# Optimization experiments

Hardware: AMD Instinct MI355X
Metric: run time of the kernel (lower is better)

The kernel has to match this reference:

```python
import jax, jax.numpy as jnp
import numpy as np

SCORE_THRESH = 0.05
NMS_THRESH = 0.5
K = 1000            # max NMS candidates (fixed for jit; padded/masked)
IMG_W, IMG_H = 1333, 800


def setup_inputs() -> dict:
    key = jax.random.key(0)
    k1, k2, k3 = jax.random.split(key, 3)
    N, C = 200000, 81
    class_logits = jax.random.normal(k1, (N, C), dtype=jnp.float32) * 2.0
    # well-formed xyxy boxes inside the image
    cxcy = jax.random.uniform(k2, (N, 2), dtype=jnp.float32) * jnp.array([IMG_W, IMG_H], jnp.float32)
    wh = jax.random.uniform(k3, (N, 2), dtype=jnp.float32) * 200.0 + 1.0
    boxes = jnp.concatenate([cxcy - wh * 0.5, cxcy + wh * 0.5], axis=-1)
    return {"class_logits": class_logits, "boxes": boxes}


def _pairwise_iou(b):
    # b: [K, 4] xyxy -> [K, K]
    area = (b[:, 2] - b[:, 0]) * (b[:, 3] - b[:, 1])
    lt = jnp.maximum(b[:, None, :2], b[None, :, :2])
    rb = jnp.minimum(b[:, None, 2:], b[None, :, 2:])
    wh = jnp.clip(rb - lt, 0.0)
    inter = wh[..., 0] * wh[..., 1]
    return inter / (area[:, None] + area[None, :] - inter + 1e-9)


def reference(class_logits, boxes):
    N, C = class_logits.shape
    prob = jax.nn.softmax(class_logits, axis=-1)            # [N, C]
    # clip_to_image (TO_REMOVE=1 convention: clamp to size-1)
    bx = jnp.stack([
        jnp.clip(boxes[:, 0], 0.0, IMG_W - 1),
        jnp.clip(boxes[:, 1], 0.0, IMG_H - 1),
        jnp.clip(boxes[:, 2], 0.0, IMG_W - 1),
        jnp.clip(boxes[:, 3], 0.0, IMG_H - 1),
    ], axis=-1)                                             # [N, 4]
    flat = prob.reshape(-1)                                 # [N*C], class = idx % C
    idx = jnp.arange(N * C)
    valid = (flat > SCORE_THRESH) & (idx % C != 0)          # fg + score threshold
    masked = jnp.where(valid, flat, -jnp.inf)
    top_scores, top_idx = jax.lax.top_k(masked, K)          # sorted descending
    prop_idx = top_idx // C
    cls = top_idx % C
    bk = bx[prop_idx]                                       # [K, 4]
    valid_k = jnp.isfinite(top_scores)
    scores_k = jnp.where(valid_k, top_scores, 0.0)
    # class-aware greedy NMS over the (sorted) top-K candidates
    conflict = (_pairwise_iou(bk) > NMS_THRESH) & (cls[:, None] == cls[None, :])
    rng = jnp.arange(K)

    def body(i, keep):
        sup = jnp.any(keep & conflict[:, i] & (rng < i))
        return keep.at[i].set(keep[i] & ~sup)

    keep = jax.lax.fori_loop(0, K, body, valid_k)
    out = jnp.concatenate([bk, scores_k[:, None]], axis=-1) * keep[:, None].astype(bk.dtype)
    return out  # [K, 5]: (x1, y1, x2, y2, score), zeroed where suppressed/invalid
```

## Files before the change

kernel.cpp:

```cpp
#include <hip/hip_runtime.h>
#include <stdint.h>
#include <math.h>

#define N_CLS    81
#define TOPK     1000
#define LISTCAP  (1u << 21)
#define CAP2     16384
#define SCORE_TH 0.05f
#define IMG_W    1333.0f
#define IMG_H    800.0f
#define GH_REP   8

#define GH_BASE  1905

#define OFF_CNT    0
#define OFF_CNT2   8
#define OFF_GH     64
#define OFF_RH     4608
#define OFF_SORTED 8704
#define MEMSET_BYTES 16704
#define OFF_SEL    16768
#define OFF_SEL2   16793984
#define OFF_BOX    16925056
#define OFF_SCORE  16941056
#define OFF_CLS    16945056
#define OFF_MASK   16949056

#define ROWS_PER_BLK 128
#define TILE_FLOATS  (ROWS_PER_BLK * N_CLS)
#define CBUF_CAP     1024

typedef unsigned long long u64;

__device__ __forceinline__ void gload_lds16(const float* g, float* l) {
    __builtin_amdgcn_global_load_lds(
        (const __attribute__((address_space(1))) unsigned int*)g,
        (__attribute__((address_space(3))) unsigned int*)l, 16, 0, 0);
}

__global__ __launch_bounds__(256) void k_pass1(
        const float* __restrict__ logits, int nrows,
        u64* __restrict__ sel, unsigned* __restrict__ cnt,
        unsigned* __restrict__ ghist) {
    __shared__ float tile[TILE_FLOATS];
    __shared__ unsigned lh[128];
    __shared__ u64 cbuf[CBUF_CAP];
    __shared__ unsigned lcnt, gbase;
    int tid = threadIdx.x, wv = tid >> 6, ln = tid & 63;
    for (int i = tid; i < 128; i += 256) lh[i] = 0;
    if (tid == 0) lcnt = 0;

    int base = blockIdx.x * ROWS_PER_BLK;
    int nr = nrows - base; if (nr > ROWS_PER_BLK) nr = ROWS_PER_BLK;
    const float* gtile = logits + (size_t)base * N_CLS;

    if (nr == ROWS_PER_BLK) {
        #pragma unroll
        for (int it = 0; it < 10; ++it) {
            int c = it * 1024 + wv * 256;
            gload_lds16(gtile + c + ln * 4, tile + c);
        }
        if (tid < TILE_FLOATS - 10240) tile[10240 + tid] = gtile[10240 + tid];
    } else {
        for (int i = tid; i < nr * N_CLS; i += 256) tile[i] = gtile[i];
    }
    __syncthreads();

    int r = tid >> 1, h = tid & 1;
    if (r < nr) {
        const int rb = r * N_CLS + h;
        float v[41];
        #pragma unroll
        for (int m = 0; m < 40; ++m) v[m] = tile[rb + 2 * m];
        v[40] = (h == 0) ? tile[rb + 80] : 0.0f;

        float mx = v[0];
        #pragma unroll
        for (int m = 1; m < 40; ++m) mx = fmaxf(mx, v[m]);
        mx = fmaxf(mx, (h == 0) ? v[40] : v[0]);
        float om = __shfl_xor(mx, 1);
        float mrow = fmaxf(mx, om);

        #pragma unroll
        for (int m = 0; m < 40; ++m) v[m] = expf(v[m] - mrow);
        v[40] = (h == 0) ? expf(v[40] - mrow) : 0.0f;

        float stk0 = 0.f, stk1 = 0.f, stk2 = 0.f, stk3 = 0.f, stk4 = 0.f;
        float S = 0.f;
        #pragma unroll
        for (int i = 0; i < 32; ++i) {
            const int b = ((i & 1) << 4) | ((i & 2) << 2) | (i & 4) |
                          ((i & 8) >> 2) | ((i & 16) >> 4);
            float x = v[b];
            if (b < 8) x += v[b + 32];
            else if (b == 8) x = (h == 0) ? x + v[40] : x;
            if (i & 1) { x = stk0 + x;
              if (i & 2) { x = stk1 + x;
                if (i & 4) { x = stk2 + x;
                  if (i & 8) { x = stk3 + x;
                    if (i & 16) { S = stk4 + x; } else stk4 = x;
                  } else stk3 = x;
                } else stk2 = x;
              } else stk1 = x;
            } else stk0 = x;
        }
        float oS = __shfl_xor(S, 1);
        float s = (h == 0) ? (S + oS) : (oS + S);

        float eth = 0.0499f * s;
        unsigned rowflat = (unsigned)(base + r) * N_CLS + (unsigned)h;
        #pragma unroll
        for (int m = 0; m < 41; ++m) {
            float e = v[m];
            if ((m + h) != 0 && e > eth) {
                float p = e / s;
                if (p > SCORE_TH) {
                    unsigned fb = __float_as_uint(p);
                    atomicAdd(&lh[(fb >> 19) - GH_BASE], 1u);
                    unsigned flat = rowflat + 2u * (unsigned)m;
                    u64 key = ((u64)fb << 32) | (u64)(0xFFFFFFu - flat);
                    unsigned pos = atomicAdd(&lcnt, 1u);
                    if (pos < CBUF_CAP) cbuf[pos] = key;
                    else { unsigned gp = atomicAdd(cnt, 1u); if (gp < LISTCAP) sel[gp] = key; }
                }
            }
        }
    }
    __syncthreads();
    unsigned* gh = ghist + (blockIdx.x & (GH_REP - 1)) * 128;
    for (int i = tid; i < 128; i += 256) {
        unsigned vv = lh[i];
        if (vv) atomicAdd(&gh[i], vv);
    }
    unsigned total = lcnt; if (total > CBUF_CAP) total = CBUF_CAP;
    if (tid == 0) gbase = atomicAdd(cnt, total);
    __syncthreads();
    unsigned gb = gbase;
    for (unsigned i = tid; i < total; i += 256) {
        unsigned gp = gb + i;
        if (gp < LISTCAP) sel[gp] = cbuf[i];
    }
}

__device__ inline int scan_coarse(const unsigned* __restrict__ ghist, unsigned* c_above) {
    unsigned cum = 0;
    for (int i = 127; i >= 0; --i) {
        unsigned c = 0;
        #pragma unroll
        for (int r = 0; r < GH_REP; r++) c += ghist[r * 128 + i];
        if (cum + c >= TOPK) { *c_above = cum; return i; }
        cum += c;
    }
    *c_above = cum;
    return -1;
}

__global__ __launch_bounds__(256) void k_refine(
        const u64* __restrict__ sel, const unsigned* __restrict__ cnt,
        const unsigned* __restrict__ ghist, unsigned* __restrict__ rhist) {
    __shared__ unsigned lh[1024];
    __shared__ int sB;
    int tid = threadIdx.x;
    for (int i = tid; i < 1024; i += 256) lh[i] = 0;
    if (tid == 0) { unsigned ca; sB = scan_coarse(ghist, &ca); }
    __syncthreads();
    int B = sB;
    if (B < 0) return;
    unsigned Bbits = (unsigned)(B + GH_BASE);
    unsigned M = *cnt; if (M > LISTCAP) M = LISTCAP;
    unsigned stride = gridDim.x * blockDim.x;
    for (unsigned i = blockIdx.x * blockDim.x + tid; i < M; i += stride) {
        unsigned bits = (unsigned)(sel[i] >> 32);
        if ((bits >> 19) == Bbits) atomicAdd(&lh[(bits >> 9) & 1023u], 1u);
    }
    __syncthreads();
    for (int i = tid; i < 1024; i += 256) {
        unsigned v = lh[i];
        if (v) atomicAdd(&rhist[i], v);
    }
}

__global__ __launch_bounds__(256) void k_select(
        const u64* __restrict__ sel, const unsigned* __restrict__ cnt,
        const unsigned* __restrict__ ghist, const unsigned* __restrict__ rhist,
        u64* __restrict__ sel2, unsigned* __restrict__ cnt2) {
    __shared__ unsigned s4[256];
    __shared__ unsigned tbs;
    int tid = threadIdx.x, ln = tid & 63;
    unsigned ps = 0;
    #pragma unroll
    for (int k = 0; k < 4; k++) ps += rhist[tid * 4 + k];
    s4[tid] = ps;
    __syncthreads();
    if (tid == 0) {
        unsigned c_above;
        int B = scan_coarse(ghist, &c_above);
        unsigned tb = 0;
        if (B >= 0) {
            unsigned cab = c_above;
            int g = -1;
            for (int i = 255; i >= 0; --i) {
                if (cab + s4[i] >= TOPK) { g = i; break; }
                cab += s4[i];
            }
            int sb = 0;
            if (g >= 0) {
                for (int i = g * 4 + 3; i >= g * 4; --i) {
                    unsigned c = rhist[i];
                    if (cab + c >= TOPK) { sb = i; break; }
                    cab += c;
                }
            }
            tb = ((unsigned)(B + GH_BASE) << 19) | ((unsigned)sb << 9);
        }
        tbs = tb;
    }
    __syncthreads();
    unsigned tb = tbs;
    unsigned M = *cnt; if (M > LISTCAP) M = LISTCAP;
    unsigned stride = gridDim.x * blockDim.x;
    for (unsigned ibase = blockIdx.x * blockDim.x; ibase < M; ibase += stride) {
        unsigned i = ibase + tid;
        bool act = (i < M);
        u64 key = act ? sel[i] : 0ull;
        bool c = act && ((unsigned)(key >> 32) >= tb);
        u64 b = __ballot(c);
        int n = __popcll(b);
        if (n == 0) continue;
        unsigned wb = 0;
        if (ln == 0) wb = atomicAdd(cnt2, (unsigned)n);
        wb = __shfl(wb, 0);
        if (c) {
            unsigned pos = wb + (unsigned)__popcll(b & ((1ull << ln) - 1ull));
            if (pos < CAP2) sel2[pos] = key;
        }
    }
}

__global__ __launch_bounds__(256) void k_rank(
        const u64* __restrict__ sel2, const unsigned* __restrict__ cnt2,
        u64* __restrict__ sorted) {
    __shared__ u64 ch[2048];
    unsigned S = *cnt2; if (S > CAP2) S = CAP2;
    if (blockIdx.x * 256u >= S) return;
    unsigned t = blockIdx.x * 256u + threadIdx.x;
    u64 my = (t < S) ? sel2[t] : 0ull;
    int r = 0;
    for (unsigned c0 = 0; c0 < S; c0 += 2048) {
        unsigned n = S - c0; if (n > 2048) n = 2048;
        __syncthreads();
        for (unsigned i = threadIdx.x; i < n; i += 256) ch[i] = sel2[c0 + i];
        __syncthreads();
        if (t < S)
            for (unsigned j = 0; j < n; j++) r += (ch[j] > my) ? 1 : 0;
    }
    if (t < S && r < TOPK) sorted[r] = my;
}

__global__ __launch_bounds__(256) void k_decode(
        const u64* __restrict__ sorted, const float* __restrict__ boxes,
        float* __restrict__ boxK, float* __restrict__ scoreK, int* __restrict__ clsK) {
    int t = blockIdx.x * blockDim.x + threadIdx.x;
    if (t >= TOPK) return;
    u64 key = sorted[t];
    if (key != 0ull) {
        float sc = __uint_as_float((unsigned)(key >> 32));
        unsigned fi = 0xFFFFFFu - (unsigned)(key & 0xFFFFFFFFull);
        unsigned prop = fi / N_CLS;
        int cls = (int)(fi - prop * N_CLS);
        const float* b = boxes + (size_t)prop * 4;
        boxK[t * 4 + 0] = fminf(fmaxf(b[0], 0.0f), IMG_W - 1.0f);
        boxK[t * 4 + 1] = fminf(fmaxf(b[1], 0.0f), IMG_H - 1.0f);
        boxK[t * 4 + 2] = fminf(fmaxf(b[2], 0.0f), IMG_W - 1.0f);
        boxK[t * 4 + 3] = fminf(fmaxf(b[3], 0.0f), IMG_H - 1.0f);
        scoreK[t] = sc;
        clsK[t] = cls;
    } else {
        boxK[t * 4 + 0] = 0.0f; boxK[t * 4 + 1] = 0.0f;
        boxK[t * 4 + 2] = 0.0f; boxK[t * 4 + 3] = 0.0f;
        scoreK[t] = 0.0f;
        clsK[t] = -1;
    }
}

__global__ __launch_bounds__(256) void k_conflict(
        const float* __restrict__ boxK, const int* __restrict__ clsK,
        u64* __restrict__ mask) {
    int t = blockIdx.x * blockDim.x + threadIdx.x;
    if (t >= TOPK * 16) return;
    int i = t >> 4, w = t & 15;
    float x1 = boxK[i * 4 + 0], y1 = boxK[i * 4 + 1];
    float x2 = boxK[i * 4 + 2], y2 = boxK[i * 4 + 3];
    int ci = clsK[i];
    float ai = (x2 - x1) * (y2 - y1);
    u64 m = 0;
    int jbase = w << 6;
    for (int jj = 0; jj < 64; jj++) {
        int j = jbase + jj;
        if (j >= TOPK) break;
        float u1 = boxK[j * 4 + 0], w1 = boxK[j * 4 + 1];
        float u2 = boxK[j * 4 + 2], w2 = boxK[j * 4 + 3];
        float aj = (u2 - u1) * (w2 - w1);
        float ww = fmaxf(fminf(x2, u2) - fmaxf(x1, u1), 0.0f);
        float hh = fmaxf(fminf(y2, w2) - fmaxf(y1, w1), 0.0f);
        float inter = ww * hh;
        float iou = inter / (ai + aj - inter + 1e-9f);
        if (iou > 0.5f && ci == clsK[j]) m |= (1ull << jj);
    }
    mask[(size_t)i * 16 + w] = m;
}

__global__ __launch_bounds__(1024) void k_nms_out(
        const u64* __restrict__ mask, const float* __restrict__ boxK,
        const float* __restrict__ scoreK, float* __restrict__ out) {
    __shared__ u64 words[16];
    __shared__ int changed;
    int tid = threadIdx.x, wv = tid >> 6, ln = tid & 63;
    bool valid = (tid < TOPK) && (scoreK[tid] > 0.0f);
    u64 row[16];
    #pragma unroll
    for (int w = 0; w < 16; w++)
        row[w] = (tid < TOPK) ? mask[(size_t)tid * 16 + w] : 0ull;
    u64 lowmask = (1ull << ln) - 1ull;
    bool keep = valid;
    for (int it = 0; it < 1024; ++it) {
        u64 b = __ballot(keep);
        if (ln == 0) words[wv] = b;
        if (tid == 0) changed = 0;
        __syncthreads();
        u64 sup = 0;
        for (int w = 0; w <= wv; w++) {
            u64 kw = words[w];
            if (w == wv) kw &= lowmask;
            sup |= row[w] & kw;
        }
        bool nk = valid && (sup == 0ull);
        if (nk != keep) changed = 1;
        keep = nk;
        __syncthreads();
        if (!changed) break;
    }
    if (tid < TOPK) {
        float x1 = boxK[tid * 4 + 0], y1 = boxK[tid * 4 + 1];
        float x2 = boxK[tid * 4 + 2], y2 = boxK[tid * 4 + 3];
        float sc = scoreK[tid];
        out[tid * 5 + 0] = keep ? x1 : 0.0f;
        out[tid * 5 + 1] = keep ? y1 : 0.0f;
        out[tid * 5 + 2] = keep ? x2 : 0.0f;
        out[tid * 5 + 3] = keep ? y2 : 0.0f;
        out[tid * 5 + 4] = keep ? sc : 0.0f;
    }
}

extern "C" void kernel_launch(void* const* d_in, const int* in_sizes, int n_in,
                              void* d_out, int out_size, void* d_ws, size_t ws_size,
                              hipStream_t stream) {
    const float* logits = (const float*)d_in[0];
    const float* boxes  = (const float*)d_in[1];
    float* out = (float*)d_out;
    int nrows = in_sizes[0] / N_CLS;

    char* w = (char*)d_ws;
    unsigned* cnt    = (unsigned*)(w + OFF_CNT);
    unsigned* cnt2   = (unsigned*)(w + OFF_CNT2);
    unsigned* ghist  = (unsigned*)(w + OFF_GH);
    unsigned* rhist  = (unsigned*)(w + OFF_RH);
    u64* sorted      = (u64*)(w + OFF_SORTED);
    u64* sel         = (u64*)(w + OFF_SEL);
    u64* sel2        = (u64*)(w + OFF_SEL2);
    float* boxK      = (float*)(w + OFF_BOX);
    float* scoreK    = (float*)(w + OFF_SCORE);
    int* clsK        = (int*)(w + OFF_CLS);
    u64* mask        = (u64*)(w + OFF_MASK);

    hipMemsetAsync(w, 0, MEMSET_BYTES, stream);

    int nblk = (nrows + ROWS_PER_BLK - 1) / ROWS_PER_BLK;
    k_pass1<<<nblk, 256, 0, stream>>>(logits, nrows, sel, cnt, ghist);
    k_refine<<<256, 256, 0, stream>>>(sel, cnt, ghist, rhist);
    k_select<<<256, 256, 0, stream>>>(sel, cnt, ghist, rhist, sel2, cnt2);
    k_rank<<<CAP2 / 256, 256, 0, stream>>>(sel2, cnt2, sorted);
    k_decode<<<(TOPK + 255) / 256, 256, 0, stream>>>(sorted, boxes, boxK, scoreK, clsK);
    k_conflict<<<(TOPK * 16 + 255) / 256, 256, 0, stream>>>(boxK, clsK, mask);
    k_nms_out<<<1, 1024, 0, stream>>>(mask, boxK, scoreK, out);
}
```

Measured before the change: 200.3 us.

## Fold threshold scans into last-block epilogues and fuse rank with decode

Pass1 now uses 64-row blocks of 128 threads and records survivors as a per-thread bitmask. A wave-wide prefix scan assigns global write positions with one atomic per wave, replacing the LDS candidate buffer. The last-arriving block of pass1 and of refine, picked with a ticket counter, computes the coarse bin and the threshold with parallel scans, so k_refine and k_select no longer rescan the histograms serially in thread 0. The rank and decode kernels are merged into one, which removes a launch and the sorted buffer. The conflict kernel now reads boxes as float4. The ticket scheme relies on threadfence ordering, and the smaller blocks roughly double the block count.

```diff
diff --git a/kernel.cpp b/kernel.cpp
--- a/kernel.cpp
+++ b/kernel.cpp
@@ -15,10 +15,14 @@
 
 #define OFF_CNT    0
 #define OFF_CNT2   8
+#define OFF_TICK1  16
+#define OFF_TICK2  20
+#define OFF_SB     24
+#define OFF_CA     28
+#define OFF_TB     32
 #define OFF_GH     64
 #define OFF_RH     4608
-#define OFF_SORTED 8704
-#define MEMSET_BYTES 16704
+#define MEMSET_BYTES 8704
 #define OFF_SEL    16768
 #define OFF_SEL2   16793984
 #define OFF_BOX    16925056
@@ -26,9 +30,8 @@
 #define OFF_CLS    16945056
 #define OFF_MASK   16949056
 
-#define ROWS_PER_BLK 128
+#define ROWS_PER_BLK 64
 #define TILE_FLOATS  (ROWS_PER_BLK * N_CLS)
-#define CBUF_CAP     1024
 
 typedef unsigned long long u64;
 
@@ -38,17 +41,21 @@
         (__attribute__((address_space(3))) unsigned int*)l, 16, 0, 0);
 }
 
-__global__ __launch_bounds__(256) void k_pass1(
+__device__ __forceinline__ unsigned agent_load_u32(const unsigned* p) {
+    return __hip_atomic_load(p, __ATOMIC_RELAXED, __HIP_MEMORY_SCOPE_AGENT);
+}
+
+__global__ __launch_bounds__(128) void k_pass1(
         const float* __restrict__ logits, int nrows,
         u64* __restrict__ sel, unsigned* __restrict__ cnt,
-        unsigned* __restrict__ ghist) {
+        unsigned* __restrict__ ghist, unsigned* __restrict__ tick,
+        int* __restrict__ psB, unsigned* __restrict__ pCA) {
     __shared__ float tile[TILE_FLOATS];
     __shared__ unsigned lh[128];
-    __shared__ u64 cbuf[CBUF_CAP];
-    __shared__ unsigned lcnt, gbase;
+    __shared__ unsigned scs[128], ssfx[128];
+    __shared__ int wB;
+    __shared__ unsigned wCA, tkt;
     int tid = threadIdx.x, wv = tid >> 6, ln = tid & 63;
-    for (int i = tid; i < 128; i += 256) lh[i] = 0;
-    if (tid == 0) lcnt = 0;
 
     int base = blockIdx.x * ROWS_PER_BLK;
     int nr = nrows - base; if (nr > ROWS_PER_BLK) nr = ROWS_PER_BLK;
@@ -57,19 +64,22 @@
     if (nr == ROWS_PER_BLK) {
         #pragma unroll
         for (int it = 0; it < 10; ++it) {
-            int c = it * 1024 + wv * 256;
+            int c = it * 512 + wv * 256;
             gload_lds16(gtile + c + ln * 4, tile + c);
         }
-        if (tid < TILE_FLOATS - 10240) tile[10240 + tid] = gtile[10240 + tid];
+        if (tid < 64) tile[5120 + tid] = gtile[5120 + tid];
     } else {
-        for (int i = tid; i < nr * N_CLS; i += 256) tile[i] = gtile[i];
-    }
+        for (int i = tid; i < nr * N_CLS; i += 128) tile[i] = gtile[i];
+    }
+    lh[tid] = 0;
     __syncthreads();
 
     int r = tid >> 1, h = tid & 1;
+    float v[41];
+    float s = 1.0f;
+    u64 bits = 0;
     if (r < nr) {
         const int rb = r * N_CLS + h;
-        float v[41];
         #pragma unroll
         for (int m = 0; m < 40; ++m) v[m] = tile[rb + 2 * m];
         v[40] = (h == 0) ? tile[rb + 80] : 0.0f;
@@ -105,118 +115,149 @@
             } else stk0 = x;
         }
         float oS = __shfl_xor(S, 1);
-        float s = (h == 0) ? (S + oS) : (oS + S);
+        s = (h == 0) ? (S + oS) : (oS + S);
 
         float eth = 0.0499f * s;
-        unsigned rowflat = (unsigned)(base + r) * N_CLS + (unsigned)h;
         #pragma unroll
         for (int m = 0; m < 41; ++m) {
             float e = v[m];
             if ((m + h) != 0 && e > eth) {
                 float p = e / s;
-                if (p > SCORE_TH) {
-                    unsigned fb = __float_as_uint(p);
-                    atomicAdd(&lh[(fb >> 19) - GH_BASE], 1u);
-                    unsigned flat = rowflat + 2u * (unsigned)m;
-                    u64 key = ((u64)fb << 32) | (u64)(0xFFFFFFu - flat);
-                    unsigned pos = atomicAdd(&lcnt, 1u);
-                    if (pos < CBUF_CAP) cbuf[pos] = key;
-                    else { unsigned gp = atomicAdd(cnt, 1u); if (gp < LISTCAP) sel[gp] = key; }
-                }
+                if (p > SCORE_TH) bits |= (1ull << m);
             }
         }
     }
-    __syncthreads();
-    unsigned* gh = ghist + (blockIdx.x & (GH_REP - 1)) * 128;
-    for (int i = tid; i < 128; i += 256) {
-        unsigned vv = lh[i];
-        if (vv) atomicAdd(&gh[i], vv);
-    }
-    unsigned total = lcnt; if (total > CBUF_CAP) total = CBUF_CAP;
-    if (tid == 0) gbase = atomicAdd(cnt, total);
-    __syncthreads();
-    unsigned gb = gbase;
-    for (unsigned i = tid; i < total; i += 256) {
-        unsigned gp = gb + i;
-        if (gp < LISTCAP) sel[gp] = cbuf[i];
-    }
-}
-
-__device__ inline int scan_coarse(const unsigned* __restrict__ ghist, unsigned* c_above) {
-    unsigned cum = 0;
-    for (int i = 127; i >= 0; --i) {
-        unsigned c = 0;
-        #pragma unroll
-        for (int r = 0; r < GH_REP; r++) c += ghist[r * 128 + i];
-        if (cum + c >= TOPK) { *c_above = cum; return i; }
-        cum += c;
-    }
-    *c_above = cum;
-    return -1;
+
+    unsigned pc = (unsigned)__popcll(bits);
+    unsigned scan = pc;
+    #pragma unroll
+    for (int off = 1; off < 64; off <<= 1) {
+        unsigned t = __shfl_up(scan, off);
+        if (ln >= off) scan += t;
+    }
+    unsigned wtotal = __shfl(scan, 63);
+    unsigned wbase = 0;
+    if (ln == 63 && wtotal) wbase = atomicAdd(cnt, wtotal);
+    wbase = __shfl(wbase, 63);
+    unsigned pos = wbase + scan - pc;
+    unsigned rowflat = (unsigned)(base + r) * N_CLS + (unsigned)h;
+    while (bits) {
+        int m = (int)(__ffsll((unsigned long long)bits) - 1);
+        bits &= bits - 1;
+        float p = v[m] / s;
+        unsigned fb = __float_as_uint(p);
+        atomicAdd(&lh[(fb >> 19) - GH_BASE], 1u);
+        if (pos < LISTCAP)
+            sel[pos] = ((u64)fb << 32) | (u64)(0xFFFFFFu - (rowflat + 2u * (unsigned)m));
+        pos++;
+    }
+
+    __syncthreads();
+    { unsigned vv = lh[tid];
+      if (vv) atomicAdd(&ghist[(blockIdx.x & (GH_REP - 1)) * 128 + tid], vv); }
+    __threadfence();
+    __syncthreads();
+    if (tid == 0) tkt = atomicAdd(tick, 1u);
+    __syncthreads();
+    if (tkt != gridDim.x - 1) return;
+
+    unsigned c = 0;
+    #pragma unroll
+    for (int rr = 0; rr < GH_REP; ++rr)
+        c += agent_load_u32(&ghist[rr * 128 + tid]);
+    scs[tid] = c; ssfx[tid] = c;
+    if (tid == 0) wB = -1;
+    __syncthreads();
+    #pragma unroll
+    for (int off = 1; off < 128; off <<= 1) {
+        unsigned a = (tid + off < 128) ? ssfx[tid + off] : 0u;
+        __syncthreads();
+        ssfx[tid] += a;
+        __syncthreads();
+    }
+    if (tid == 0) wCA = ssfx[0];
+    __syncthreads();
+    unsigned incl = ssfx[tid], excl = incl - scs[tid];
+    if (excl < TOPK && incl >= TOPK) { wB = tid; wCA = excl; }
+    __syncthreads();
+    if (tid == 0) { *psB = wB; *pCA = wCA; }
 }
 
 __global__ __launch_bounds__(256) void k_refine(
         const u64* __restrict__ sel, const unsigned* __restrict__ cnt,
-        const unsigned* __restrict__ ghist, unsigned* __restrict__ rhist) {
+        unsigned* __restrict__ rhist, unsigned* __restrict__ tick,
+        const int* __restrict__ psB, const unsigned* __restrict__ pCA,
+        unsigned* __restrict__ ptb) {
     __shared__ unsigned lh[1024];
-    __shared__ int sB;
+    __shared__ unsigned rbin[1024];
+    __shared__ unsigned sgrp[256], ssfx[256];
+    __shared__ int wg;
+    __shared__ unsigned wcab, tkt;
     int tid = threadIdx.x;
-    for (int i = tid; i < 1024; i += 256) lh[i] = 0;
-    if (tid == 0) { unsigned ca; sB = scan_coarse(ghist, &ca); }
-    __syncthreads();
-    int B = sB;
-    if (B < 0) return;
-    unsigned Bbits = (unsigned)(B + GH_BASE);
-    unsigned M = *cnt; if (M > LISTCAP) M = LISTCAP;
-    unsigned stride = gridDim.x * blockDim.x;
-    for (unsigned i = blockIdx.x * blockDim.x + tid; i < M; i += stride) {
-        unsigned bits = (unsigned)(sel[i] >> 32);
-        if ((bits >> 19) == Bbits) atomicAdd(&lh[(bits >> 9) & 1023u], 1u);
-    }
-    __syncthreads();
-    for (int i = tid; i < 1024; i += 256) {
-        unsigned v = lh[i];
-        if (v) atomicAdd(&rhist[i], v);
+    int B = *psB;
+    if (B >= 0) {
+        for (int i = tid; i < 1024; i += 256) lh[i] = 0;
+        __syncthreads();
+        unsigned Bbits = (unsigned)(B + GH_BASE);
+        unsigned M = *cnt; if (M > LISTCAP) M = LISTCAP;
+        unsigned stride = gridDim.x * blockDim.x;
+        for (unsigned i = blockIdx.x * blockDim.x + tid; i < M; i += stride) {
+            unsigned bv = (unsigned)(sel[i] >> 32);
+            if ((bv >> 19) == Bbits) atomicAdd(&lh[(bv >> 9) & 1023u], 1u);
+        }
+        __syncthreads();
+        for (int i = tid; i < 1024; i += 256) {
+            unsigned vv = lh[i];
+            if (vv) atomicAdd(&rhist[i], vv);
+        }
+    }
+    __threadfence();
+    __syncthreads();
+    if (tid == 0) tkt = atomicAdd(tick, 1u);
+    __syncthreads();
+    if (tkt != gridDim.x - 1) return;
+
+    if (B < 0) { if (tid == 0) *ptb = 0u; return; }
+    unsigned CA = *pCA;
+    unsigned gsum = 0;
+    #pragma unroll
+    for (int k = 0; k < 4; ++k) {
+        unsigned bv = agent_load_u32(&rhist[tid * 4 + k]);
+        rbin[tid * 4 + k] = bv; gsum += bv;
+    }
+    sgrp[tid] = gsum; ssfx[tid] = gsum;
+    if (tid == 0) wg = -1;
+    __syncthreads();
+    #pragma unroll
+    for (int off = 1; off < 256; off <<= 1) {
+        unsigned a = (tid + off < 256) ? ssfx[tid + off] : 0u;
+        __syncthreads();
+        ssfx[tid] += a;
+        __syncthreads();
+    }
+    unsigned incl = ssfx[tid], excl = incl - sgrp[tid];
+    if (CA + excl < TOPK && CA + incl >= TOPK) { wg = tid; wcab = CA + excl; }
+    __syncthreads();
+    if (tid == 0) {
+        int g = wg; unsigned sb = 0;
+        if (g >= 0) {
+            unsigned cab = wcab;
+            for (int i = g * 4 + 3; i >= g * 4; --i) {
+                unsigned cc = rbin[i];
+                if (cab + cc >= TOPK) { sb = (unsigned)i; break; }
+                cab += cc;
+            }
+        }
+        *ptb = ((unsigned)(B + GH_BASE) << 19) | (sb << 9);
     }
 }
 
 __global__ __launch_bounds__(256) void k_select(
         const u64* __restrict__ sel, const unsigned* __restrict__ cnt,
-        const unsigned* __restrict__ ghist, const unsigned* __restrict__ rhist,
+        const unsigned* __restrict__ ptb,
         u64* __restrict__ sel2, unsigned* __restrict__ cnt2) {
-    __shared__ unsigned s4[256];
-    __shared__ unsigned tbs;
     int tid = threadIdx.x, ln = tid & 63;
-    unsigned ps = 0;
-    #pragma unroll
-    for (int k = 0; k < 4; k++) ps += rhist[tid * 4 + k];
-    s4[tid] = ps;
-    __syncthreads();
-    if (tid == 0) {
-        unsigned c_above;
-        int B = scan_coarse(ghist, &c_above);
-        unsigned tb = 0;
-        if (B >= 0) {
-            unsigned cab = c_above;
-            int g = -1;
-            for (int i = 255; i >= 0; --i) {
-                if (cab + s4[i] >= TOPK) { g = i; break; }
-                cab += s4[i];
-            }
-            int sb = 0;
-            if (g >= 0) {
-                for (int i = g * 4 + 3; i >= g * 4; --i) {
-                    unsigned c = rhist[i];
-                    if (cab + c >= TOPK) { sb = i; break; }
-                    cab += c;
-                }
-            }
-            tb = ((unsigned)(B + GH_BASE) << 19) | ((unsigned)sb << 9);
-        }
-        tbs = tb;
-    }
-    __syncthreads();
-    unsigned tb = tbs;
+    unsigned tb = *ptb;
     unsigned M = *cnt; if (M > LISTCAP) M = LISTCAP;
     unsigned stride = gridDim.x * blockDim.x;
     for (unsigned ibase = blockIdx.x * blockDim.x; ibase < M; ibase += stride) {
@@ -237,13 +278,21 @@
     }
 }
 
-__global__ __launch_bounds__(256) void k_rank(
+__global__ __launch_bounds__(256) void k_rank_decode(
         const u64* __restrict__ sel2, const unsigned* __restrict__ cnt2,
-        u64* __restrict__ sorted) {
+        const float* __restrict__ boxes,
+        float* __restrict__ boxK, float* __restrict__ scoreK, int* __restrict__ clsK) {
     __shared__ u64 ch[2048];
     unsigned S = *cnt2; if (S > CAP2) S = CAP2;
-    if (blockIdx.x * 256u >= S) return;
     unsigned t = blockIdx.x * 256u + threadIdx.x;
+    if (blockIdx.x * 256u >= S) {
+        if (t < TOPK) {
+            boxK[t * 4 + 0] = 0.0f; boxK[t * 4 + 1] = 0.0f;
+            boxK[t * 4 + 2] = 0.0f; boxK[t * 4 + 3] = 0.0f;
+            scoreK[t] = 0.0f; clsK[t] = -1;
+        }
+        return;
+    }
     u64 my = (t < S) ? sel2[t] : 0ull;
     int r = 0;
     for (unsigned c0 = 0; c0 < S; c0 += 2048) {
@@ -254,32 +303,24 @@
         if (t < S)
             for (unsigned j = 0; j < n; j++) r += (ch[j] > my) ? 1 : 0;
     }
-    if (t < S && r < TOPK) sorted[r] = my;
-}
-
-__global__ __launch_bounds__(256) void k_decode(
-        const u64* __restrict__ sorted, const float* __restrict__ boxes,
-        float* __restrict__ boxK, float* __restrict__ scoreK, int* __restrict__ clsK) {
-    int t = blockIdx.x * blockDim.x + threadIdx.x;
-    if (t >= TOPK) return;
-    u64 key = sorted[t];
-    if (key != 0ull) {
-        float sc = __uint_as_float((unsigned)(key >> 32));
-        unsigned fi = 0xFFFFFFu - (unsigned)(key & 0xFFFFFFFFull);
-        unsigned prop = fi / N_CLS;
-        int cls = (int)(fi - prop * N_CLS);
-        const float* b = boxes + (size_t)prop * 4;
-        boxK[t * 4 + 0] = fminf(fmaxf(b[0], 0.0f), IMG_W - 1.0f);
-        boxK[t * 4 + 1] = fminf(fmaxf(b[1], 0.0f), IMG_H - 1.0f);
-        boxK[t * 4 + 2] = fminf(fmaxf(b[2], 0.0f), IMG_W - 1.0f);
-        boxK[t * 4 + 3] = fminf(fmaxf(b[3], 0.0f), IMG_H - 1.0f);
-        scoreK[t] = sc;
-        clsK[t] = cls;
-    } else {
+    if (t < S) {
+        if (r < TOPK) {
+            float sc = __uint_as_float((unsigned)(my >> 32));
+            unsigned fi = 0xFFFFFFu - (unsigned)(my & 0xFFFFFFFFull);
+            unsigned prop = fi / N_CLS;
+            int cls = (int)(fi - prop * N_CLS);
+            const float* b = boxes + (size_t)prop * 4;
+            boxK[r * 4 + 0] = fminf(fmaxf(b[0], 0.0f), IMG_W - 1.0f);
+            boxK[r * 4 + 1] = fminf(fmaxf(b[1], 0.0f), IMG_H - 1.0f);
+            boxK[r * 4 + 2] = fminf(fmaxf(b[2], 0.0f), IMG_W - 1.0f);
+            boxK[r * 4 + 3] = fminf(fmaxf(b[3], 0.0f), IMG_H - 1.0f);
+            scoreK[r] = sc;
+            clsK[r] = cls;
+        }
+    } else if (t < TOPK) {
         boxK[t * 4 + 0] = 0.0f; boxK[t * 4 + 1] = 0.0f;
         boxK[t * 4 + 2] = 0.0f; boxK[t * 4 + 3] = 0.0f;
-        scoreK[t] = 0.0f;
-        clsK[t] = -1;
+        scoreK[t] = 0.0f; clsK[t] = -1;
     }
 }
 
@@ -289,20 +330,19 @@
     int t = blockIdx.x * blockDim.x + threadIdx.x;
     if (t >= TOPK * 16) return;
     int i = t >> 4, w = t & 15;
-    float x1 = boxK[i * 4 + 0], y1 = boxK[i * 4 + 1];
-    float x2 = boxK[i * 4 + 2], y2 = boxK[i * 4 + 3];
+    const float4* b4 = (const float4*)boxK;
+    float4 bi = b4[i];
     int ci = clsK[i];
-    float ai = (x2 - x1) * (y2 - y1);
+    float ai = (bi.z - bi.x) * (bi.w - bi.y);
     u64 m = 0;
     int jbase = w << 6;
     for (int jj = 0; jj < 64; jj++) {
         int j = jbase + jj;
         if (j >= TOPK) break;
-        float u1 = boxK[j * 4 + 0], w1 = boxK[j * 4 + 1];
-        float u2 = boxK[j * 4 + 2], w2 = boxK[j * 4 + 3];
-        float aj = (u2 - u1) * (w2 - w1);
-        float ww = fmaxf(fminf(x2, u2) - fmaxf(x1, u1), 0.0f);
-        float hh = fmaxf(fminf(y2, w2) - fmaxf(y1, w1), 0.0f);
+        float4 bj = b4[j];
+        float aj = (bj.z - bj.x) * (bj.w - bj.y);
+        float ww = fmaxf(fminf(bi.z, bj.z) - fmaxf(bi.x, bj.x), 0.0f);
+        float hh = fmaxf(fminf(bi.w, bj.w) - fmaxf(bi.y, bj.y), 0.0f);
         float inter = ww * hh;
         float iou = inter / (ai + aj - inter + 1e-9f);
         if (iou > 0.5f && ci == clsK[j]) m |= (1ull << jj);
@@ -363,9 +403,13 @@
     char* w = (char*)d_ws;
     unsigned* cnt    = (unsigned*)(w + OFF_CNT);
     unsigned* cnt2   = (unsigned*)(w + OFF_CNT2);
+    unsigned* tick1  = (unsigned*)(w + OFF_TICK1);
+    unsigned* tick2  = (unsigned*)(w + OFF_TICK2);
+    int*      psB    = (int*)(w + OFF_SB);
+    unsigned* pCA    = (unsigned*)(w + OFF_CA);
+    unsigned* ptb    = (unsigned*)(w + OFF_TB);
     unsigned* ghist  = (unsigned*)(w + OFF_GH);
     unsigned* rhist  = (unsigned*)(w + OFF_RH);
-    u64* sorted      = (u64*)(w + OFF_SORTED);
     u64* sel         = (u64*)(w + OFF_SEL);
     u64* sel2        = (u64*)(w + OFF_SEL2);
     float* boxK      = (float*)(w + OFF_BOX);
@@ -376,11 +420,10 @@
     hipMemsetAsync(w, 0, MEMSET_BYTES, stream);
 
     int nblk = (nrows + ROWS_PER_BLK - 1) / ROWS_PER_BLK;
-    k_pass1<<<nblk, 256, 0, stream>>>(logits, nrows, sel, cnt, ghist);
-    k_refine<<<256, 256, 0, stream>>>(sel, cnt, ghist, rhist);
-    k_select<<<256, 256, 0, stream>>>(sel, cnt, ghist, rhist, sel2, cnt2);
-    k_rank<<<CAP2 / 256, 256, 0, stream>>>(sel2, cnt2, sorted);
-    k_decode<<<(TOPK + 255) / 256, 256, 0, stream>>>(sorted, boxes, boxK, scoreK, clsK);
+    k_pass1<<<nblk, 128, 0, stream>>>(logits, nrows, sel, cnt, ghist, tick1, psB, pCA);
+    k_refine<<<256, 256, 0, stream>>>(sel, cnt, rhist, tick2, psB, pCA, ptb);
+    k_select<<<256, 256, 0, stream>>>(sel, cnt, ptb, sel2, cnt2);
+    k_rank_decode<<<CAP2 / 256, 256, 0, stream>>>(sel2, cnt2, boxes, boxK, scoreK, clsK);
     k_conflict<<<(TOPK * 16 + 255) / 256, 256, 0, stream>>>(boxK, clsK, mask);
     k_nms_out<<<1, 1024, 0, stream>>>(mask, boxK, scoreK, out);
 }
```

Measured after the change: 464.3 us. 2.32x slower.
